# Performance work log

Hardware: AMD Instinct MI355X
Metric: run time of the kernel (lower is better)

Reference implementation:

```python
import jax, jax.numpy as jnp
import numpy as np

N_NODES = 100000
N_EDGES = 1600000
DIM = 64
NEG_SLOPE = 0.2  # DGL GATConv default
BN_EPS = 1e-5


def setup_inputs() -> dict:
    key = jax.random.key(0)
    ks = jax.random.split(key, 16)
    d = {}
    d["node_weight"] = jax.random.normal(ks[0], (N_NODES, DIM), jnp.float32)
    d["edge_weight"] = jax.random.normal(ks[1], (N_EDGES,), jnp.float32)  # unused in forward (faithful to source)
    d["src"] = jax.random.randint(ks[2], (N_EDGES,), 0, N_NODES)
    d["dst"] = jax.random.randint(ks[3], (N_EDGES,), 0, N_NODES)
    i = 4
    scale = 1.0 / np.sqrt(DIM)
    for l in (1, 2, 3):
        d[f"W{l}"] = jax.random.normal(ks[i], (DIM, DIM), jnp.float32) * scale; i += 1
        d[f"al{l}"] = jax.random.normal(ks[i], (DIM,), jnp.float32) * 0.1; i += 1
        d[f"ar{l}"] = jax.random.normal(ks[i], (DIM,), jnp.float32) * 0.1; i += 1
        d[f"b{l}"] = jnp.zeros((DIM,), jnp.float32)
        d[f"g{l}"] = jnp.ones((DIM,), jnp.float32)
        d[f"beta{l}"] = jnp.zeros((DIM,), jnp.float32)
    return d


def gat_layer(h, src, dst, W, al, ar, b):
    # DGL GATConv, 1 head: project, edge attention, per-dst softmax, scatter-add
    feat = h @ W                                  # [N, D]
    el = feat @ al                                # [N]
    er = feat @ ar                                # [N]
    e = jax.nn.leaky_relu(el[src] + er[dst], NEG_SLOPE)   # [E]
    m = jax.ops.segment_max(e, dst, num_segments=N_NODES)  # per-dst max
    ex = jnp.exp(e - m[dst])
    s = jax.ops.segment_sum(ex, dst, num_segments=N_NODES)
    alpha = ex / s[dst]                           # edge softmax
    out = jax.ops.segment_sum(alpha[:, None] * feat[src], dst, num_segments=N_NODES)
    return out + b


def batchnorm(h, g, beta):
    # BatchNorm1d in training mode: batch stats, biased variance
    mu = jnp.mean(h, axis=0)
    var = jnp.mean(jnp.square(h - mu), axis=0)
    return (h - mu) * jax.lax.rsqrt(var + BN_EPS) * g + beta


def reference(node_weight, edge_weight, src, dst,
              W1, al1, ar1, b1, g1, beta1,
              W2, al2, ar2, b2, g2, beta2,
              W3, al3, ar3, b3, g3, beta3):
    # dropout is identity in eval mode
    h = gat_layer(node_weight, src, dst, W1, al1, ar1, b1)
    h = jax.nn.elu(batchnorm(h, g1, beta1))
    h = gat_layer(h, src, dst, W2, al2, ar2, b2)
    h = jax.nn.elu(batchnorm(h, g2, beta2))
    h = gat_layer(h, src, dst, W3, al3, ar3, b3)
    h = batchnorm(h, g3, beta3)
    return h
```

## Files before the change

kernel.cpp:

```cpp
#include <hip/hip_runtime.h>
#include <hip/hip_bf16.h>
#include <math.h>

#define DIM 64
#define BSHIFT 9
#define BNODES 512
#define MAXB 256
#define EPT 8
#define CHUNK 2048

typedef __attribute__((ext_vector_type(8))) short bf16x8;
typedef __attribute__((ext_vector_type(4))) float f32x4;

__device__ __forceinline__ short f2bf(float x) {
    union { __hip_bfloat16 b; short s; } u;
    u.b = __float2bfloat16(x);
    return u.s;
}
__device__ __forceinline__ float bf2f(short s) {
    return __uint_as_float(((unsigned)(unsigned short)s) << 16);
}


__global__ void bin_count_kernel(const int* __restrict__ dst, int* __restrict__ bucket_cnt, int E) {
    __shared__ int h[MAXB];
    int t = threadIdx.x;
    h[t] = 0;
    __syncthreads();
    for (int i = blockIdx.x * blockDim.x + t; i < E; i += gridDim.x * blockDim.x)
        atomicAdd(&h[dst[i] >> BSHIFT], 1);
    __syncthreads();
    if (h[t]) atomicAdd(&bucket_cnt[t], h[t]);
}

__global__ void bucket_scan_kernel(const int* __restrict__ bucket_cnt,
                                   int* __restrict__ bucket_off, int* __restrict__ bucket_fill) {
    __shared__ int s[MAXB];
    int t = threadIdx.x;
    int v = bucket_cnt[t];
    s[t] = v;
    __syncthreads();
    for (int off = 1; off < MAXB; off <<= 1) {
        int x = (t >= off) ? s[t - off] : 0;
        __syncthreads();
        s[t] += x;
        __syncthreads();
    }
    bucket_off[t] = s[t] - v;
    bucket_fill[t] = 0;
}

__global__ __launch_bounds__(256) void bin_scatter_kernel(
    const int* __restrict__ src, const int* __restrict__ dst,
    const int* __restrict__ bucket_off, int* __restrict__ bucket_fill,
    unsigned long long* __restrict__ binned, int E) {
    __shared__ int lcnt[MAXB];
    __shared__ int lbase[MAXB];
    int t = threadIdx.x;
    lcnt[t] = 0;
    __syncthreads();
    int base = blockIdx.x * CHUNK;
    unsigned long long pair[EPT];
    int slot[EPT];
#pragma unroll
    for (int j = 0; j < EPT; j++) {
        int idx = base + j * 256 + t;
        if (idx < E) {
            int s = src[idx], d = dst[idx];
            pair[j] = ((unsigned long long)(unsigned)d << 32) | (unsigned)s;
            slot[j] = atomicAdd(&lcnt[d >> BSHIFT], 1);
        } else {
            slot[j] = -1;
        }
    }
    __syncthreads();
    int c = lcnt[t];
    if (c) lbase[t] = atomicAdd(&bucket_fill[t], c);
    __syncthreads();
#pragma unroll
    for (int j = 0; j < EPT; j++) {
        if (slot[j] >= 0) {
            int b = (int)(pair[j] >> 32) >> BSHIFT;
            binned[(size_t)bucket_off[b] + lbase[b] + slot[j]] = pair[j];
        }
    }
}

__global__ __launch_bounds__(256) void node_count_kernel(
    const unsigned long long* __restrict__ binned, const int* __restrict__ bucket_off,
    const int* __restrict__ bucket_cnt, int* __restrict__ counts, int N) {
    __shared__ int cnt[BNODES];
    int b = blockIdx.x, t = threadIdx.x;
    for (int i = t; i < BNODES; i += 256) cnt[i] = 0;
    __syncthreads();
    int s0 = bucket_off[b], c = bucket_cnt[b];
    for (int i = t; i < c; i += 256) {
        int d = (int)(binned[(size_t)s0 + i] >> 32);
        atomicAdd(&cnt[d & (BNODES - 1)], 1);
    }
    __syncthreads();
    int nbase = b << BSHIFT;
    for (int i = t; i < BNODES; i += 256)
        if (nbase + i < N) counts[nbase + i] = cnt[i];
}

__global__ void scan1_kernel(const int* __restrict__ counts, int* __restrict__ excl,
                             int* __restrict__ blk_sums, int n) {
    __shared__ int sdata[256];
    int t = threadIdx.x;
    int base = blockIdx.x * 1024 + t * 4;
    int v0 = (base + 0 < n) ? counts[base + 0] : 0;
    int v1 = (base + 1 < n) ? counts[base + 1] : 0;
    int v2 = (base + 2 < n) ? counts[base + 2] : 0;
    int v3 = (base + 3 < n) ? counts[base + 3] : 0;
    int tsum = v0 + v1 + v2 + v3;
    sdata[t] = tsum;
    __syncthreads();
    for (int off = 1; off < 256; off <<= 1) {
        int x = (t >= off) ? sdata[t - off] : 0;
        __syncthreads();
        sdata[t] += x;
        __syncthreads();
    }
    int run = sdata[t] - tsum;
    if (base + 0 < n) excl[base + 0] = run; run += v0;
    if (base + 1 < n) excl[base + 1] = run; run += v1;
    if (base + 2 < n) excl[base + 2] = run; run += v2;
    if (base + 3 < n) excl[base + 3] = run;
    if (t == 255) blk_sums[blockIdx.x] = sdata[255];
}

__global__ void scan2_kernel(int* __restrict__ blk_sums, int nb) {
    __shared__ int s[128];
    int t = threadIdx.x;
    s[t] = (t < nb) ? blk_sums[t] : 0;
    __syncthreads();
    for (int off = 1; off < 128; off <<= 1) {
        int x = (t >= off) ? s[t - off] : 0;
        __syncthreads();
        s[t] += x;
        __syncthreads();
    }
    if (t < nb) blk_sums[t] = (t > 0) ? s[t - 1] : 0;
}

__global__ void scan3_kernel(int* __restrict__ excl, const int* __restrict__ blk_sums,
                             int n, int total) {
    int i = blockIdx.x * blockDim.x + threadIdx.x;
    if (i < n) excl[i] += blk_sums[i >> 10];
    if (i == 0) excl[n] = total;
}

__global__ __launch_bounds__(256) void final_scatter_kernel(
    const unsigned long long* __restrict__ binned, const int* __restrict__ bucket_off,
    const int* __restrict__ bucket_cnt, const int* __restrict__ row_ptr,
    int* __restrict__ src_sorted, int N) {
    __shared__ int fill[BNODES];
    int b = blockIdx.x, t = threadIdx.x;
    for (int i = t; i < BNODES; i += 256) fill[i] = 0;
    __syncthreads();
    int s0 = bucket_off[b], c = bucket_cnt[b];
    for (int i = t; i < c; i += 256) {
        unsigned long long p = binned[(size_t)s0 + i];
        int d = (int)(p >> 32);
        int pos = row_ptr[d] + atomicAdd(&fill[d & (BNODES - 1)], 1);
        src_sorted[pos] = (int)(p & 0xffffffffu);
    }
}


__global__ __launch_bounds__(256) void gemm64_mfma_kernel(
    const float* __restrict__ h, const float* __restrict__ W,
    const float* __restrict__ al, const float* __restrict__ ar,
    const float* __restrict__ stats, const float* __restrict__ g,
    const float* __restrict__ beta, int do_bn, float invN,
    __hip_bfloat16* __restrict__ feat, float* __restrict__ el, float* __restrict__ er,
    int n) {
    int t = threadIdx.x;
    int lane = t & 63;
    int li = lane & 15;
    int quad = lane >> 4;
    int wv = t >> 6;

    bf16x8 b_hi[2][4], b_lo[2][4];
#pragma unroll
    for (int ks = 0; ks < 2; ks++)
#pragma unroll
        for (int nt = 0; nt < 4; nt++) {
#pragma unroll
            for (int j = 0; j < 8; j++) {
                float w = W[(ks * 32 + quad * 8 + j) * 64 + nt * 16 + li];
                short hi = f2bf(w);
                b_hi[ks][nt][j] = hi;
                b_lo[ks][nt][j] = f2bf(w - bf2f(hi));
            }
        }
    float alv[4], arv[4];
#pragma unroll
    for (int nt = 0; nt < 4; nt++) { alv[nt] = al[nt * 16 + li]; arv[nt] = ar[nt * 16 + li]; }

    float sc[2][8], sh[2][8];
    if (do_bn) {
#pragma unroll
        for (int ks = 0; ks < 2; ks++)
#pragma unroll
            for (int j = 0; j < 8; j++) {
                int k = ks * 32 + quad * 8 + j;
                float mu = stats[k] * invN;
                float var = fmaf(-mu, mu, stats[64 + k] * invN);
                float inv = rsqrtf(var + 1e-5f) * g[k];
                sc[ks][j] = inv;
                sh[ks][j] = beta[k] - mu * inv;
            }
    }

    int ntiles = (n + 15) >> 4;
    for (int tile = blockIdx.x * 4 + wv; tile < ntiles; tile += gridDim.x * 4) {
        int m0 = tile << 4;
        int rrow = m0 + li;
        const float* rowp = h + (size_t)((rrow < n) ? rrow : (n - 1)) * 64;
        bf16x8 a_hi[2], a_lo[2];
#pragma unroll
        for (int ks = 0; ks < 2; ks++) {
            float4 v0 = *(const float4*)(rowp + ks * 32 + quad * 8);
            float4 v1 = *(const float4*)(rowp + ks * 32 + quad * 8 + 4);
            float x[8] = {v0.x, v0.y, v0.z, v0.w, v1.x, v1.y, v1.z, v1.w};
#pragma unroll
            for (int j = 0; j < 8; j++) {
                float v = x[j];
                if (do_bn) {
                    v = fmaf(v, sc[ks][j], sh[ks][j]);
                    if (v < 0.f) v = expm1f(v);
                }
                short hi = f2bf(v);
                a_hi[ks][j] = hi;
                a_lo[ks][j] = f2bf(v - bf2f(hi));
            }
        }
        f32x4 acc[4];
#pragma unroll
        for (int nt = 0; nt < 4; nt++) acc[nt] = (f32x4){0.f, 0.f, 0.f, 0.f};
#pragma unroll
        for (int ks = 0; ks < 2; ks++)
#pragma unroll
            for (int nt = 0; nt < 4; nt++) {
                acc[nt] = __builtin_amdgcn_mfma_f32_16x16x32_bf16(a_hi[ks], b_hi[ks][nt], acc[nt], 0, 0, 0);
                acc[nt] = __builtin_amdgcn_mfma_f32_16x16x32_bf16(a_lo[ks], b_hi[ks][nt], acc[nt], 0, 0, 0);
                acc[nt] = __builtin_amdgcn_mfma_f32_16x16x32_bf16(a_hi[ks], b_lo[ks][nt], acc[nt], 0, 0, 0);
            }
#pragma unroll
        for (int nt = 0; nt < 4; nt++)
#pragma unroll
            for (int reg = 0; reg < 4; reg++) {
                int wrow = m0 + quad * 4 + reg;
                if (wrow < n) {
                    union { __hip_bfloat16 b; short s; } u;
                    u.s = f2bf(acc[nt][reg]);
                    feat[(size_t)wrow * 64 + nt * 16 + li] = u.b;
                }
            }
        float pl[4], pr[4];
#pragma unroll
        for (int reg = 0; reg < 4; reg++) {
            float l = 0.f, r = 0.f;
#pragma unroll
            for (int nt = 0; nt < 4; nt++) {
                l = fmaf(acc[nt][reg], alv[nt], l);
                r = fmaf(acc[nt][reg], arv[nt], r);
            }
#pragma unroll
            for (int off = 1; off < 16; off <<= 1) {
                l += __shfl_xor(l, off, 64);
                r += __shfl_xor(r, off, 64);
            }
            pl[reg] = l; pr[reg] = r;
        }
        int row = m0 + quad * 4;
        if (li == 0 && row < n)          { el[row] = pl[0]; er[row] = pr[0]; }
        else if (li == 1 && row + 1 < n) { el[row + 1] = pl[1]; er[row + 1] = pr[1]; }
        else if (li == 2 && row + 2 < n) { el[row + 2] = pl[2]; er[row + 2] = pr[2]; }
        else if (li == 3 && row + 3 < n) { el[row + 3] = pl[3]; er[row + 3] = pr[3]; }
    }
}

__global__ __launch_bounds__(256) void attn_kernel(
    const int* __restrict__ row_ptr, const int* __restrict__ src_sorted,
    const float* __restrict__ el, const float* __restrict__ er,
    float* __restrict__ ebuf, int n) {
    int t = threadIdx.x;
    int li = t & 15;
    int node = blockIdx.x * 16 + (t >> 4);
    if (node >= n) return;
    int start = row_ptr[node], end = row_ptr[node + 1];
    float er_n = er[node];

    float m = -INFINITY, s = 0.f;
    for (int i = start + li; i < end; i += 16) {
        float v = el[src_sorted[i]] + er_n;
        v = (v > 0.f) ? v : 0.2f * v;
        ebuf[i] = v;
        float mn = fmaxf(m, v);
        s = s * __expf(m - mn) + __expf(v - mn);
        m = mn;
    }
#pragma unroll
    for (int off = 8; off; off >>= 1) {
        float mo = __shfl_xor(m, off, 64);
        float so = __shfl_xor(s, off, 64);
        float mn = fmaxf(m, mo);
        float sa = (m == -INFINITY) ? 0.f : s * __expf(m - mn);
        float sb = (mo == -INFINITY) ? 0.f : so * __expf(mo - mn);
        s = sa + sb;
        m = mn;
    }
    float inv_s = (s > 0.f) ? 1.f / s : 0.f;
    for (int i = start + li; i < end; i += 16) {
        ebuf[i] = __expf(ebuf[i] - m) * inv_s;
    }
}

__global__ __launch_bounds__(256) void aggregate_kernel(
    const int* __restrict__ row_ptr, const int* __restrict__ src_sorted,
    const float* __restrict__ alpha, const __hip_bfloat16* __restrict__ feat,
    const float* __restrict__ bias, float* __restrict__ out, int n) {
    int t = threadIdx.x, lane = t & 63;
    int q = lane >> 3;
    int li = lane & 7;
    int node = blockIdx.x * 4 + (t >> 6);
    if (node >= n) return;
    int start = row_ptr[node], end = row_ptr[node + 1];
    const uint4* featv = (const uint4*)feat;

    float a0 = 0.f, a1 = 0.f, a2 = 0.f, a3 = 0.f, a4 = 0.f, a5 = 0.f, a6 = 0.f, a7 = 0.f;
    int i = start;
    for (; i + 8 <= end; i += 8) {
        int idx = i + q;
        float a = alpha[idx];
        int sn = src_sorted[idx];
        uint4 p = featv[(size_t)sn * 8 + li];
        a0 = fmaf(a, __uint_as_float(p.x << 16), a0);
        a1 = fmaf(a, __uint_as_float(p.x & 0xffff0000u), a1);
        a2 = fmaf(a, __uint_as_float(p.y << 16), a2);
        a3 = fmaf(a, __uint_as_float(p.y & 0xffff0000u), a3);
        a4 = fmaf(a, __uint_as_float(p.z << 16), a4);
        a5 = fmaf(a, __uint_as_float(p.z & 0xffff0000u), a5);
        a6 = fmaf(a, __uint_as_float(p.w << 16), a6);
        a7 = fmaf(a, __uint_as_float(p.w & 0xffff0000u), a7);
    }
    if (i < end) {
        int idx = i + q;
        bool valid = idx < end;
        int idc = valid ? idx : end - 1;
        float a = valid ? alpha[idc] : 0.f;
        int sn = src_sorted[idc];
        uint4 p = featv[(size_t)sn * 8 + li];
        a0 = fmaf(a, __uint_as_float(p.x << 16), a0);
        a1 = fmaf(a, __uint_as_float(p.x & 0xffff0000u), a1);
        a2 = fmaf(a, __uint_as_float(p.y << 16), a2);
        a3 = fmaf(a, __uint_as_float(p.y & 0xffff0000u), a3);
        a4 = fmaf(a, __uint_as_float(p.z << 16), a4);
        a5 = fmaf(a, __uint_as_float(p.z & 0xffff0000u), a5);
        a6 = fmaf(a, __uint_as_float(p.w << 16), a6);
        a7 = fmaf(a, __uint_as_float(p.w & 0xffff0000u), a7);
    }
#pragma unroll
    for (int off = 8; off <= 32; off <<= 1) {
        a0 += __shfl_xor(a0, off, 64);
        a1 += __shfl_xor(a1, off, 64);
        a2 += __shfl_xor(a2, off, 64);
        a3 += __shfl_xor(a3, off, 64);
        a4 += __shfl_xor(a4, off, 64);
        a5 += __shfl_xor(a5, off, 64);
        a6 += __shfl_xor(a6, off, 64);
        a7 += __shfl_xor(a7, off, 64);
    }
    if (q == 0) {
        const float4* bv = (const float4*)bias;
        float4 b0 = bv[li * 2], b1 = bv[li * 2 + 1];
        float4 o0 = {a0 + b0.x, a1 + b0.y, a2 + b0.z, a3 + b0.w};
        float4 o1 = {a4 + b1.x, a5 + b1.y, a6 + b1.z, a7 + b1.w};
        float4* op = (float4*)(out + (size_t)node * 64 + li * 8);
        op[0] = o0;
        op[1] = o1;
    }
}

__global__ __launch_bounds__(256) void bn_stats_kernel(const float* __restrict__ h,
                                                       float* __restrict__ stats, int n) {
    __shared__ float ls[256], lss[256];
    int t = threadIdx.x, lane = t & 63;
    int w = blockIdx.x * 4 + (t >> 6);
    int stride = gridDim.x * 4;
    float s = 0.f, ss = 0.f;
    for (int row = w; row < n; row += stride) {
        float v = h[(size_t)row * DIM + lane];
        s += v;
        ss = fmaf(v, v, ss);
    }
    ls[t] = s; lss[t] = ss;
    __syncthreads();
    if (t < 64) {
        float a = ls[t] + ls[t + 64] + ls[t + 128] + ls[t + 192];
        float b = lss[t] + lss[t + 64] + lss[t + 128] + lss[t + 192];
        atomicAdd(&stats[t], a);
        atomicAdd(&stats[64 + t], b);
    }
}

__global__ void bn_apply_kernel(float* __restrict__ h, const float* __restrict__ stats,
                                const float* __restrict__ g, const float* __restrict__ beta,
                                int n, int do_elu) {
    int i = blockIdx.x * blockDim.x + threadIdx.x;
    int total = n * DIM;
    int stride = gridDim.x * blockDim.x;
    float invN = 1.f / (float)n;
    for (; i < total; i += stride) {
        int c = i & 63;
        float mu = stats[c] * invN;
        float var = fmaf(-mu, mu, stats[DIM + c] * invN);
        float x = (h[i] - mu) * rsqrtf(var + 1e-5f) * g[c] + beta[c];
        if (do_elu && x < 0.f) x = expm1f(x);
        h[i] = x;
    }
}


extern "C" void kernel_launch(void* const* d_in, const int* in_sizes, int n_in,
                              void* d_out, int out_size, void* d_ws, size_t ws_size,
                              hipStream_t stream) {
    const float* nw = (const float*)d_in[0];
    const int* src = (const int*)d_in[2];
    const int* dst = (const int*)d_in[3];
    const int N = in_sizes[0] / DIM;
    const int E = in_sizes[2];
    const float invN = 1.f / (float)N;
    const int nbuck = (N + BNODES - 1) >> BSHIFT;

    char* ws = (char*)d_ws;
    size_t off = 0;
    auto alloc = [&](size_t bytes) -> void* {
        void* p = ws + off;
        off += (bytes + 255) & ~(size_t)255;
        return p;
    };
    int* counts       = (int*)alloc((size_t)N * 4);
    int* row_ptr      = (int*)alloc(((size_t)N + 1) * 4);
    int* blk_sums     = (int*)alloc(512);
    int* bucket_cnt   = (int*)alloc(MAXB * 4);
    int* bucket_off   = (int*)alloc(MAXB * 4);
    int* bucket_fill  = (int*)alloc(MAXB * 4);
    unsigned long long* binned = (unsigned long long*)alloc((size_t)E * 8);
    int* src_sorted   = (int*)alloc((size_t)E * 4);
    float* ebuf       = (float*)alloc((size_t)E * 4);
    float* el         = (float*)alloc((size_t)N * 4);
    float* er         = (float*)alloc((size_t)N * 4);
    __hip_bfloat16* feat = (__hip_bfloat16*)alloc((size_t)N * DIM * 2);
    float* hbuf       = (float*)alloc((size_t)N * DIM * 4);
    float* stats      = (float*)alloc(512);

    int nb = (N + 1023) / 1024;

    hipMemsetAsync(bucket_cnt, 0, MAXB * 4, stream);
    bin_count_kernel<<<256, 256, 0, stream>>>(dst, bucket_cnt, E);
    bucket_scan_kernel<<<1, MAXB, 0, stream>>>(bucket_cnt, bucket_off, bucket_fill);
    bin_scatter_kernel<<<(E + CHUNK - 1) / CHUNK, 256, 0, stream>>>(
        src, dst, bucket_off, bucket_fill, binned, E);
    node_count_kernel<<<nbuck, 256, 0, stream>>>(binned, bucket_off, bucket_cnt, counts, N);
    scan1_kernel<<<nb, 256, 0, stream>>>(counts, row_ptr, blk_sums, N);
    scan2_kernel<<<1, 128, 0, stream>>>(blk_sums, nb);
    scan3_kernel<<<(N + 255) / 256, 256, 0, stream>>>(row_ptr, blk_sums, N, E);
    final_scatter_kernel<<<nbuck, 256, 0, stream>>>(binned, bucket_off, bucket_cnt,
                                                    row_ptr, src_sorted, N);

    for (int l = 0; l < 3; l++) {
        const float* W    = (const float*)d_in[4 + 6 * l];
        const float* al   = (const float*)d_in[5 + 6 * l];
        const float* ar   = (const float*)d_in[6 + 6 * l];
        const float* b    = (const float*)d_in[7 + 6 * l];
        const float* g    = (const float*)d_in[8 + 6 * l];
        const float* beta = (const float*)d_in[9 + 6 * l];
        const float* hin = (l == 0) ? nw : hbuf;
        float* hout = (l == 2) ? (float*)d_out : hbuf;

        gemm64_mfma_kernel<<<1024, 256, 0, stream>>>(
            hin, W, al, ar, stats,
            (l == 0) ? al : (const float*)d_in[8 + 6 * (l - 1)],
            (l == 0) ? al : (const float*)d_in[9 + 6 * (l - 1)],
            (l > 0) ? 1 : 0, invN,
            feat, el, er, N);
        attn_kernel<<<(N + 15) / 16, 256, 0, stream>>>(row_ptr, src_sorted, el, er, ebuf, N);
        aggregate_kernel<<<(N + 3) / 4, 256, 0, stream>>>(row_ptr, src_sorted, ebuf,
                                                          feat, b, hout, N);
        hipMemsetAsync(stats, 0, 512, stream);
        bn_stats_kernel<<<512, 256, 0, stream>>>(hout, stats, N);
    }
    bn_apply_kernel<<<2048, 256, 0, stream>>>((float*)d_out, stats,
                                              (const float*)d_in[8 + 12],
                                              (const float*)d_in[9 + 12],
                                              N, 0);
}
```

Before: 517.2 us.

## Fuse edge softmax, aggregation and BN stats into one kernel with bf16 intermediates

Merges the attention, aggregation and batch-norm statistics kernels into a single persistent per-node kernel. Each wavefront computes the softmax for its node in registers and uses it directly, so the edge buffer round trip goes away. The kernel also accumulates the column sums and sums of squares in shared memory before doing the global atomics. Hidden activations between layers are now stored as bf16 and read back by the GEMM, and some loads and stores become nontemporal. These changes cut global memory traffic and launch count, at the cost of lower precision in the intermediate activations.

```diff
diff --git a/kernel.cpp b/kernel.cpp
--- a/kernel.cpp
+++ b/kernel.cpp
@@ -11,6 +11,7 @@
 
 typedef __attribute__((ext_vector_type(8))) short bf16x8;
 typedef __attribute__((ext_vector_type(4))) float f32x4;
+typedef __attribute__((ext_vector_type(4))) unsigned int u32x4;
 
 __device__ __forceinline__ short f2bf(float x) {
     union { __hip_bfloat16 b; short s; } u;
@@ -170,10 +171,10 @@
 
 
 __global__ __launch_bounds__(256) void gemm64_mfma_kernel(
-    const float* __restrict__ h, const float* __restrict__ W,
+    const void* __restrict__ hraw, const float* __restrict__ W,
     const float* __restrict__ al, const float* __restrict__ ar,
     const float* __restrict__ stats, const float* __restrict__ g,
-    const float* __restrict__ beta, int do_bn, float invN,
+    const float* __restrict__ beta, int do_bn, int in_bf16, float invN,
     __hip_bfloat16* __restrict__ feat, float* __restrict__ el, float* __restrict__ er,
     int n) {
     int t = threadIdx.x;
@@ -218,13 +219,25 @@
     for (int tile = blockIdx.x * 4 + wv; tile < ntiles; tile += gridDim.x * 4) {
         int m0 = tile << 4;
         int rrow = m0 + li;
-        const float* rowp = h + (size_t)((rrow < n) ? rrow : (n - 1)) * 64;
+        int crow = (rrow < n) ? rrow : (n - 1);
         bf16x8 a_hi[2], a_lo[2];
 #pragma unroll
         for (int ks = 0; ks < 2; ks++) {
-            float4 v0 = *(const float4*)(rowp + ks * 32 + quad * 8);
-            float4 v1 = *(const float4*)(rowp + ks * 32 + quad * 8 + 4);
-            float x[8] = {v0.x, v0.y, v0.z, v0.w, v1.x, v1.y, v1.z, v1.w};
+            float x[8];
+            if (in_bf16) {
+                const u32x4* rp = (const u32x4*)((const __hip_bfloat16*)hraw + (size_t)crow * 64 + ks * 32 + quad * 8);
+                u32x4 pv = __builtin_nontemporal_load(rp);
+                x[0] = __uint_as_float(pv[0] << 16); x[1] = __uint_as_float(pv[0] & 0xffff0000u);
+                x[2] = __uint_as_float(pv[1] << 16); x[3] = __uint_as_float(pv[1] & 0xffff0000u);
+                x[4] = __uint_as_float(pv[2] << 16); x[5] = __uint_as_float(pv[2] & 0xffff0000u);
+                x[6] = __uint_as_float(pv[3] << 16); x[7] = __uint_as_float(pv[3] & 0xffff0000u);
+            } else {
+                const float* rowp = (const float*)hraw + (size_t)crow * 64 + ks * 32 + quad * 8;
+                f32x4 v0 = __builtin_nontemporal_load((const f32x4*)rowp);
+                f32x4 v1 = __builtin_nontemporal_load((const f32x4*)(rowp + 4));
+                x[0] = v0[0]; x[1] = v0[1]; x[2] = v0[2]; x[3] = v0[3];
+                x[4] = v1[0]; x[5] = v1[1]; x[6] = v1[2]; x[7] = v1[3];
+            }
 #pragma unroll
             for (int j = 0; j < 8; j++) {
                 float v = x[j];
@@ -283,128 +296,180 @@
     }
 }
 
-__global__ __launch_bounds__(256) void attn_kernel(
+template<int OUT_BF16>
+__global__ __launch_bounds__(256) void fused_layer_kernel(
     const int* __restrict__ row_ptr, const int* __restrict__ src_sorted,
     const float* __restrict__ el, const float* __restrict__ er,
-    float* __restrict__ ebuf, int n) {
-    int t = threadIdx.x;
-    int li = t & 15;
-    int node = blockIdx.x * 16 + (t >> 4);
-    if (node >= n) return;
-    int start = row_ptr[node], end = row_ptr[node + 1];
-    float er_n = er[node];
-
-    float m = -INFINITY, s = 0.f;
-    for (int i = start + li; i < end; i += 16) {
-        float v = el[src_sorted[i]] + er_n;
-        v = (v > 0.f) ? v : 0.2f * v;
-        ebuf[i] = v;
-        float mn = fmaxf(m, v);
-        s = s * __expf(m - mn) + __expf(v - mn);
-        m = mn;
-    }
-#pragma unroll
-    for (int off = 8; off; off >>= 1) {
-        float mo = __shfl_xor(m, off, 64);
-        float so = __shfl_xor(s, off, 64);
-        float mn = fmaxf(m, mo);
-        float sa = (m == -INFINITY) ? 0.f : s * __expf(m - mn);
-        float sb = (mo == -INFINITY) ? 0.f : so * __expf(mo - mn);
-        s = sa + sb;
-        m = mn;
-    }
-    float inv_s = (s > 0.f) ? 1.f / s : 0.f;
-    for (int i = start + li; i < end; i += 16) {
-        ebuf[i] = __expf(ebuf[i] - m) * inv_s;
-    }
-}
-
-__global__ __launch_bounds__(256) void aggregate_kernel(
-    const int* __restrict__ row_ptr, const int* __restrict__ src_sorted,
-    const float* __restrict__ alpha, const __hip_bfloat16* __restrict__ feat,
-    const float* __restrict__ bias, float* __restrict__ out, int n) {
-    int t = threadIdx.x, lane = t & 63;
+    const __hip_bfloat16* __restrict__ feat, const float* __restrict__ bias,
+    void* __restrict__ out, float* __restrict__ stats, int n) {
+    __shared__ float colsum[128];
+    int t = threadIdx.x, lane = t & 63, wv = t >> 6;
     int q = lane >> 3;
     int li = lane & 7;
-    int node = blockIdx.x * 4 + (t >> 6);
-    if (node >= n) return;
-    int start = row_ptr[node], end = row_ptr[node + 1];
     const uint4* featv = (const uint4*)feat;
-
-    float a0 = 0.f, a1 = 0.f, a2 = 0.f, a3 = 0.f, a4 = 0.f, a5 = 0.f, a6 = 0.f, a7 = 0.f;
-    int i = start;
-    for (; i + 8 <= end; i += 8) {
-        int idx = i + q;
-        float a = alpha[idx];
-        int sn = src_sorted[idx];
-        uint4 p = featv[(size_t)sn * 8 + li];
-        a0 = fmaf(a, __uint_as_float(p.x << 16), a0);
-        a1 = fmaf(a, __uint_as_float(p.x & 0xffff0000u), a1);
-        a2 = fmaf(a, __uint_as_float(p.y << 16), a2);
-        a3 = fmaf(a, __uint_as_float(p.y & 0xffff0000u), a3);
-        a4 = fmaf(a, __uint_as_float(p.z << 16), a4);
-        a5 = fmaf(a, __uint_as_float(p.z & 0xffff0000u), a5);
-        a6 = fmaf(a, __uint_as_float(p.w << 16), a6);
-        a7 = fmaf(a, __uint_as_float(p.w & 0xffff0000u), a7);
-    }
-    if (i < end) {
-        int idx = i + q;
-        bool valid = idx < end;
-        int idc = valid ? idx : end - 1;
-        float a = valid ? alpha[idc] : 0.f;
-        int sn = src_sorted[idc];
-        uint4 p = featv[(size_t)sn * 8 + li];
-        a0 = fmaf(a, __uint_as_float(p.x << 16), a0);
-        a1 = fmaf(a, __uint_as_float(p.x & 0xffff0000u), a1);
-        a2 = fmaf(a, __uint_as_float(p.y << 16), a2);
-        a3 = fmaf(a, __uint_as_float(p.y & 0xffff0000u), a3);
-        a4 = fmaf(a, __uint_as_float(p.z << 16), a4);
-        a5 = fmaf(a, __uint_as_float(p.z & 0xffff0000u), a5);
-        a6 = fmaf(a, __uint_as_float(p.w << 16), a6);
-        a7 = fmaf(a, __uint_as_float(p.w & 0xffff0000u), a7);
-    }
-#pragma unroll
-    for (int off = 8; off <= 32; off <<= 1) {
-        a0 += __shfl_xor(a0, off, 64);
-        a1 += __shfl_xor(a1, off, 64);
-        a2 += __shfl_xor(a2, off, 64);
-        a3 += __shfl_xor(a3, off, 64);
-        a4 += __shfl_xor(a4, off, 64);
-        a5 += __shfl_xor(a5, off, 64);
-        a6 += __shfl_xor(a6, off, 64);
-        a7 += __shfl_xor(a7, off, 64);
-    }
+    float b0[8];
+#pragma unroll
+    for (int j = 0; j < 8; j++) b0[j] = bias[li * 8 + j];
+    float st_s[8], st_q[8];
+#pragma unroll
+    for (int j = 0; j < 8; j++) { st_s[j] = 0.f; st_q[j] = 0.f; }
+
+    for (int node = blockIdx.x * 4 + wv; node < n; node += gridDim.x * 4) {
+        int start = row_ptr[node], end = row_ptr[node + 1];
+        int deg = end - start;
+        float er_n = er[node];
+        float a0 = 0.f, a1 = 0.f, a2 = 0.f, a3 = 0.f, a4 = 0.f, a5 = 0.f, a6 = 0.f, a7 = 0.f;
+
+        if (deg <= 64) {
+            int sv = 0;
+            float ev = -INFINITY;
+            if (lane < deg) {
+                sv = __builtin_nontemporal_load(src_sorted + start + lane);
+                float v = el[sv] + er_n;
+                ev = (v > 0.f) ? v : 0.2f * v;
+            }
+            float m = ev;
+#pragma unroll
+            for (int off = 1; off < 64; off <<= 1) m = fmaxf(m, __shfl_xor(m, off, 64));
+            float sum = (lane < deg) ? __expf(ev - m) : 0.f;
+#pragma unroll
+            for (int off = 1; off < 64; off <<= 1) sum += __shfl_xor(sum, off, 64);
+            float inv_s = (sum > 0.f) ? 1.f / sum : 0.f;
+
+            int nit = (deg + 7) >> 3;
+            int it = 0;
+            for (; it + 2 <= nit; it += 2) {
+                int o1 = it * 8 + q, o2 = o1 + 8;
+                bool v2 = o2 < deg;
+                int s1 = __shfl(sv, o1, 64);
+                int s2 = __shfl(sv, v2 ? o2 : o1, 64);
+                float e1 = __shfl(ev, o1, 64);
+                float e2 = __shfl(ev, v2 ? o2 : o1, 64);
+                uint4 p1 = featv[(size_t)s1 * 8 + li];
+                uint4 p2 = featv[(size_t)s2 * 8 + li];
+                float w1 = __expf(e1 - m) * inv_s;
+                float w2 = v2 ? __expf(e2 - m) * inv_s : 0.f;
+                a0 = fmaf(w1, __uint_as_float(p1.x << 16), a0);
+                a1 = fmaf(w1, __uint_as_float(p1.x & 0xffff0000u), a1);
+                a2 = fmaf(w1, __uint_as_float(p1.y << 16), a2);
+                a3 = fmaf(w1, __uint_as_float(p1.y & 0xffff0000u), a3);
+                a4 = fmaf(w1, __uint_as_float(p1.z << 16), a4);
+                a5 = fmaf(w1, __uint_as_float(p1.z & 0xffff0000u), a5);
+                a6 = fmaf(w1, __uint_as_float(p1.w << 16), a6);
+                a7 = fmaf(w1, __uint_as_float(p1.w & 0xffff0000u), a7);
+                a0 = fmaf(w2, __uint_as_float(p2.x << 16), a0);
+                a1 = fmaf(w2, __uint_as_float(p2.x & 0xffff0000u), a1);
+                a2 = fmaf(w2, __uint_as_float(p2.y << 16), a2);
+                a3 = fmaf(w2, __uint_as_float(p2.y & 0xffff0000u), a3);
+                a4 = fmaf(w2, __uint_as_float(p2.z << 16), a4);
+                a5 = fmaf(w2, __uint_as_float(p2.z & 0xffff0000u), a5);
+                a6 = fmaf(w2, __uint_as_float(p2.w << 16), a6);
+                a7 = fmaf(w2, __uint_as_float(p2.w & 0xffff0000u), a7);
+            }
+            if (it < nit) {
+                int o = it * 8 + q;
+                bool valid = o < deg;
+                int oc = valid ? o : 0;
+                int s1 = __shfl(sv, oc, 64);
+                float e1 = __shfl(ev, oc, 64);
+                uint4 p = featv[(size_t)s1 * 8 + li];
+                float w1 = valid ? __expf(e1 - m) * inv_s : 0.f;
+                a0 = fmaf(w1, __uint_as_float(p.x << 16), a0);
+                a1 = fmaf(w1, __uint_as_float(p.x & 0xffff0000u), a1);
+                a2 = fmaf(w1, __uint_as_float(p.y << 16), a2);
+                a3 = fmaf(w1, __uint_as_float(p.y & 0xffff0000u), a3);
+                a4 = fmaf(w1, __uint_as_float(p.z << 16), a4);
+                a5 = fmaf(w1, __uint_as_float(p.z & 0xffff0000u), a5);
+                a6 = fmaf(w1, __uint_as_float(p.w << 16), a6);
+                a7 = fmaf(w1, __uint_as_float(p.w & 0xffff0000u), a7);
+            }
+        } else {
+            float mm = -INFINITY, ss = 0.f;
+            for (int i = start + lane; i < end; i += 64) {
+                int sn = src_sorted[i];
+                float v = el[sn] + er_n;
+                v = (v > 0.f) ? v : 0.2f * v;
+                float mn = fmaxf(mm, v);
+                ss = ss * __expf(mm - mn) + __expf(v - mn);
+                mm = mn;
+            }
+#pragma unroll
+            for (int off = 1; off < 64; off <<= 1) {
+                float mo = __shfl_xor(mm, off, 64);
+                float so = __shfl_xor(ss, off, 64);
+                float mn = fmaxf(mm, mo);
+                float sa = (mm == -INFINITY) ? 0.f : ss * __expf(mm - mn);
+                float sb = (mo == -INFINITY) ? 0.f : so * __expf(mo - mn);
+                ss = sa + sb;
+                mm = mn;
+            }
+            float m = mm;
+            float inv_s = (ss > 0.f) ? 1.f / ss : 0.f;
+            for (int i = start; i < end; i += 8) {
+                int o = i + q;
+                bool valid = o < end;
+                int oc = valid ? o : end - 1;
+                int sn = src_sorted[oc];
+                float v = el[sn] + er_n;
+                v = (v > 0.f) ? v : 0.2f * v;
+                float w1 = valid ? __expf(v - m) * inv_s : 0.f;
+                uint4 p = featv[(size_t)sn * 8 + li];
+                a0 = fmaf(w1, __uint_as_float(p.x << 16), a0);
+                a1 = fmaf(w1, __uint_as_float(p.x & 0xffff0000u), a1);
+                a2 = fmaf(w1, __uint_as_float(p.y << 16), a2);
+                a3 = fmaf(w1, __uint_as_float(p.y & 0xffff0000u), a3);
+                a4 = fmaf(w1, __uint_as_float(p.z << 16), a4);
+                a5 = fmaf(w1, __uint_as_float(p.z & 0xffff0000u), a5);
+                a6 = fmaf(w1, __uint_as_float(p.w << 16), a6);
+                a7 = fmaf(w1, __uint_as_float(p.w & 0xffff0000u), a7);
+            }
+        }
+#pragma unroll
+        for (int off = 8; off <= 32; off <<= 1) {
+            a0 += __shfl_xor(a0, off, 64);
+            a1 += __shfl_xor(a1, off, 64);
+            a2 += __shfl_xor(a2, off, 64);
+            a3 += __shfl_xor(a3, off, 64);
+            a4 += __shfl_xor(a4, off, 64);
+            a5 += __shfl_xor(a5, off, 64);
+            a6 += __shfl_xor(a6, off, 64);
+            a7 += __shfl_xor(a7, off, 64);
+        }
+        if (q == 0) {
+            float o_[8] = {a0 + b0[0], a1 + b0[1], a2 + b0[2], a3 + b0[3],
+                           a4 + b0[4], a5 + b0[5], a6 + b0[6], a7 + b0[7]};
+#pragma unroll
+            for (int j = 0; j < 8; j++) {
+                st_s[j] += o_[j];
+                st_q[j] = fmaf(o_[j], o_[j], st_q[j]);
+            }
+            if (OUT_BF16) {
+                u32x4 pk;
+                pk[0] = ((unsigned)(unsigned short)f2bf(o_[0])) | ((unsigned)(unsigned short)f2bf(o_[1]) << 16);
+                pk[1] = ((unsigned)(unsigned short)f2bf(o_[2])) | ((unsigned)(unsigned short)f2bf(o_[3]) << 16);
+                pk[2] = ((unsigned)(unsigned short)f2bf(o_[4])) | ((unsigned)(unsigned short)f2bf(o_[5]) << 16);
+                pk[3] = ((unsigned)(unsigned short)f2bf(o_[6])) | ((unsigned)(unsigned short)f2bf(o_[7]) << 16);
+                __builtin_nontemporal_store(pk, (u32x4*)((__hip_bfloat16*)out + (size_t)node * 64 + li * 8));
+            } else {
+                f32x4 v0 = {o_[0], o_[1], o_[2], o_[3]};
+                f32x4 v1 = {o_[4], o_[5], o_[6], o_[7]};
+                f32x4* op = (f32x4*)((float*)out + (size_t)node * 64 + li * 8);
+                __builtin_nontemporal_store(v0, op);
+                __builtin_nontemporal_store(v1, op + 1);
+            }
+        }
+    }
+    if (t < 128) colsum[t] = 0.f;
+    __syncthreads();
     if (q == 0) {
-        const float4* bv = (const float4*)bias;
-        float4 b0 = bv[li * 2], b1 = bv[li * 2 + 1];
-        float4 o0 = {a0 + b0.x, a1 + b0.y, a2 + b0.z, a3 + b0.w};
-        float4 o1 = {a4 + b1.x, a5 + b1.y, a6 + b1.z, a7 + b1.w};
-        float4* op = (float4*)(out + (size_t)node * 64 + li * 8);
-        op[0] = o0;
-        op[1] = o1;
-    }
-}
-
-__global__ __launch_bounds__(256) void bn_stats_kernel(const float* __restrict__ h,
-                                                       float* __restrict__ stats, int n) {
-    __shared__ float ls[256], lss[256];
-    int t = threadIdx.x, lane = t & 63;
-    int w = blockIdx.x * 4 + (t >> 6);
-    int stride = gridDim.x * 4;
-    float s = 0.f, ss = 0.f;
-    for (int row = w; row < n; row += stride) {
-        float v = h[(size_t)row * DIM + lane];
-        s += v;
-        ss = fmaf(v, v, ss);
-    }
-    ls[t] = s; lss[t] = ss;
-    __syncthreads();
-    if (t < 64) {
-        float a = ls[t] + ls[t + 64] + ls[t + 128] + ls[t + 192];
-        float b = lss[t] + lss[t + 64] + lss[t + 128] + lss[t + 192];
-        atomicAdd(&stats[t], a);
-        atomicAdd(&stats[64 + t], b);
-    }
+#pragma unroll
+        for (int j = 0; j < 8; j++) {
+            atomicAdd(&colsum[li * 8 + j], st_s[j]);
+            atomicAdd(&colsum[64 + li * 8 + j], st_q[j]);
+        }
+    }
+    __syncthreads();
+    if (t < 128) atomicAdd(&stats[t], colsum[t]);
 }
 
 __global__ void bn_apply_kernel(float* __restrict__ h, const float* __restrict__ stats,
@@ -451,11 +516,10 @@
     int* bucket_fill  = (int*)alloc(MAXB * 4);
     unsigned long long* binned = (unsigned long long*)alloc((size_t)E * 8);
     int* src_sorted   = (int*)alloc((size_t)E * 4);
-    float* ebuf       = (float*)alloc((size_t)E * 4);
     float* el         = (float*)alloc((size_t)N * 4);
     float* er         = (float*)alloc((size_t)N * 4);
     __hip_bfloat16* feat = (__hip_bfloat16*)alloc((size_t)N * DIM * 2);
-    float* hbuf       = (float*)alloc((size_t)N * DIM * 4);
+    __hip_bfloat16* hbuf = (__hip_bfloat16*)alloc((size_t)N * DIM * 2);
     float* stats      = (float*)alloc(512);
 
     int nb = (N + 1023) / 1024;
@@ -477,22 +541,21 @@
         const float* al   = (const float*)d_in[5 + 6 * l];
         const float* ar   = (const float*)d_in[6 + 6 * l];
         const float* b    = (const float*)d_in[7 + 6 * l];
-        const float* g    = (const float*)d_in[8 + 6 * l];
-        const float* beta = (const float*)d_in[9 + 6 * l];
-        const float* hin = (l == 0) ? nw : hbuf;
-        float* hout = (l == 2) ? (float*)d_out : hbuf;
 
         gemm64_mfma_kernel<<<1024, 256, 0, stream>>>(
-            hin, W, al, ar, stats,
+            (l == 0) ? (const void*)nw : (const void*)hbuf, W, al, ar, stats,
             (l == 0) ? al : (const float*)d_in[8 + 6 * (l - 1)],
             (l == 0) ? al : (const float*)d_in[9 + 6 * (l - 1)],
-            (l > 0) ? 1 : 0, invN,
+            (l > 0) ? 1 : 0, (l > 0) ? 1 : 0, invN,
             feat, el, er, N);
-        attn_kernel<<<(N + 15) / 16, 256, 0, stream>>>(row_ptr, src_sorted, el, er, ebuf, N);
-        aggregate_kernel<<<(N + 3) / 4, 256, 0, stream>>>(row_ptr, src_sorted, ebuf,
-                                                          feat, b, hout, N);
         hipMemsetAsync(stats, 0, 512, stream);
-        bn_stats_kernel<<<512, 256, 0, stream>>>(hout, stats, N);
+        if (l < 2) {
+            fused_layer_kernel<1><<<4096, 256, 0, stream>>>(
+                row_ptr, src_sorted, el, er, feat, b, (void*)hbuf, stats, N);
+        } else {
+            fused_layer_kernel<0><<<4096, 256, 0, stream>>>(
+                row_ptr, src_sorted, el, er, feat, b, d_out, stats, N);
+        }
     }
     bn_apply_kernel<<<2048, 256, 0, stream>>>((float*)d_out, stats,
                                               (const float*)d_in[8 + 12],
```

Result: slower. 656.9 us (+27.0%).

## Fuse CSR build into one bucket kernel, fuse BN stats into aggregation, bf16 hidden buffers

Applied to the files above, without the earlier changes.

Replaces the node-count, three-pass scan and final-scatter kernels with a single per-bucket kernel that counts, scans locally and scatters, using the bucket offsets as global bases. The aggregation kernel becomes grid-strided and accumulates the batchnorm column sums and squares itself, which removes the separate stats pass over the hidden activations. Intermediate hidden activations are stored in bf16 instead of fp32, halving that traffic, and several loads and stores are marked nontemporal. The risks are reduced precision in the intermediates and atomic contention on the stats accumulators.

```diff
diff --git a/kernel.cpp b/kernel.cpp
--- a/kernel.cpp
+++ b/kernel.cpp
@@ -11,6 +11,7 @@
 
 typedef __attribute__((ext_vector_type(8))) short bf16x8;
 typedef __attribute__((ext_vector_type(4))) float f32x4;
+typedef __attribute__((ext_vector_type(4))) unsigned int u32x4;
 
 __device__ __forceinline__ short f2bf(float x) {
     union { __hip_bfloat16 b; short s; } u;
@@ -86,12 +87,15 @@
     }
 }
 
-__global__ __launch_bounds__(256) void node_count_kernel(
+__global__ __launch_bounds__(256) void bucket_csr_kernel(
     const unsigned long long* __restrict__ binned, const int* __restrict__ bucket_off,
-    const int* __restrict__ bucket_cnt, int* __restrict__ counts, int N) {
+    const int* __restrict__ bucket_cnt, int* __restrict__ row_ptr,
+    int* __restrict__ src_sorted, int N, int E) {
     __shared__ int cnt[BNODES];
+    __shared__ int base[BNODES];
+    __shared__ int sdata[256];
     int b = blockIdx.x, t = threadIdx.x;
-    for (int i = t; i < BNODES; i += 256) cnt[i] = 0;
+    cnt[t] = 0; cnt[t + 256] = 0;
     __syncthreads();
     int s0 = bucket_off[b], c = bucket_cnt[b];
     for (int i = t; i < c; i += 256) {
@@ -99,21 +103,8 @@
         atomicAdd(&cnt[d & (BNODES - 1)], 1);
     }
     __syncthreads();
-    int nbase = b << BSHIFT;
-    for (int i = t; i < BNODES; i += 256)
-        if (nbase + i < N) counts[nbase + i] = cnt[i];
-}
-
-__global__ void scan1_kernel(const int* __restrict__ counts, int* __restrict__ excl,
-                             int* __restrict__ blk_sums, int n) {
-    __shared__ int sdata[256];
-    int t = threadIdx.x;
-    int base = blockIdx.x * 1024 + t * 4;
-    int v0 = (base + 0 < n) ? counts[base + 0] : 0;
-    int v1 = (base + 1 < n) ? counts[base + 1] : 0;
-    int v2 = (base + 2 < n) ? counts[base + 2] : 0;
-    int v3 = (base + 3 < n) ? counts[base + 3] : 0;
-    int tsum = v0 + v1 + v2 + v3;
+    int v0 = cnt[2 * t], v1 = cnt[2 * t + 1];
+    int tsum = v0 + v1;
     sdata[t] = tsum;
     __syncthreads();
     for (int off = 1; off < 256; off <<= 1) {
@@ -123,57 +114,28 @@
         __syncthreads();
     }
     int run = sdata[t] - tsum;
-    if (base + 0 < n) excl[base + 0] = run; run += v0;
-    if (base + 1 < n) excl[base + 1] = run; run += v1;
-    if (base + 2 < n) excl[base + 2] = run; run += v2;
-    if (base + 3 < n) excl[base + 3] = run;
-    if (t == 255) blk_sums[blockIdx.x] = sdata[255];
-}
-
-__global__ void scan2_kernel(int* __restrict__ blk_sums, int nb) {
-    __shared__ int s[128];
-    int t = threadIdx.x;
-    s[t] = (t < nb) ? blk_sums[t] : 0;
-    __syncthreads();
-    for (int off = 1; off < 128; off <<= 1) {
-        int x = (t >= off) ? s[t - off] : 0;
-        __syncthreads();
-        s[t] += x;
-        __syncthreads();
-    }
-    if (t < nb) blk_sums[t] = (t > 0) ? s[t - 1] : 0;
-}
-
-__global__ void scan3_kernel(int* __restrict__ excl, const int* __restrict__ blk_sums,
-                             int n, int total) {
-    int i = blockIdx.x * blockDim.x + threadIdx.x;
-    if (i < n) excl[i] += blk_sums[i >> 10];
-    if (i == 0) excl[n] = total;
-}
-
-__global__ __launch_bounds__(256) void final_scatter_kernel(
-    const unsigned long long* __restrict__ binned, const int* __restrict__ bucket_off,
-    const int* __restrict__ bucket_cnt, const int* __restrict__ row_ptr,
-    int* __restrict__ src_sorted, int N) {
-    __shared__ int fill[BNODES];
-    int b = blockIdx.x, t = threadIdx.x;
-    for (int i = t; i < BNODES; i += 256) fill[i] = 0;
-    __syncthreads();
-    int s0 = bucket_off[b], c = bucket_cnt[b];
+    base[2 * t] = s0 + run;
+    base[2 * t + 1] = s0 + run + v0;
+    int nbase = b << BSHIFT;
+    if (nbase + 2 * t < N)     row_ptr[nbase + 2 * t]     = s0 + run;
+    if (nbase + 2 * t + 1 < N) row_ptr[nbase + 2 * t + 1] = s0 + run + v0;
+    if (b == 0 && t == 0) row_ptr[N] = E;
+    cnt[2 * t] = 0; cnt[2 * t + 1] = 0;
+    __syncthreads();
     for (int i = t; i < c; i += 256) {
         unsigned long long p = binned[(size_t)s0 + i];
-        int d = (int)(p >> 32);
-        int pos = row_ptr[d] + atomicAdd(&fill[d & (BNODES - 1)], 1);
+        int d = (int)(p >> 32) & (BNODES - 1);
+        int pos = base[d] + atomicAdd(&cnt[d], 1);
         src_sorted[pos] = (int)(p & 0xffffffffu);
     }
 }
 
 
 __global__ __launch_bounds__(256) void gemm64_mfma_kernel(
-    const float* __restrict__ h, const float* __restrict__ W,
+    const void* __restrict__ hraw, const float* __restrict__ W,
     const float* __restrict__ al, const float* __restrict__ ar,
     const float* __restrict__ stats, const float* __restrict__ g,
-    const float* __restrict__ beta, int do_bn, float invN,
+    const float* __restrict__ beta, int do_bn, int in_bf16, float invN,
     __hip_bfloat16* __restrict__ feat, float* __restrict__ el, float* __restrict__ er,
     int n) {
     int t = threadIdx.x;
@@ -218,13 +180,25 @@
     for (int tile = blockIdx.x * 4 + wv; tile < ntiles; tile += gridDim.x * 4) {
         int m0 = tile << 4;
         int rrow = m0 + li;
-        const float* rowp = h + (size_t)((rrow < n) ? rrow : (n - 1)) * 64;
+        int crow = (rrow < n) ? rrow : (n - 1);
         bf16x8 a_hi[2], a_lo[2];
 #pragma unroll
         for (int ks = 0; ks < 2; ks++) {
-            float4 v0 = *(const float4*)(rowp + ks * 32 + quad * 8);
-            float4 v1 = *(const float4*)(rowp + ks * 32 + quad * 8 + 4);
-            float x[8] = {v0.x, v0.y, v0.z, v0.w, v1.x, v1.y, v1.z, v1.w};
+            float x[8];
+            if (in_bf16) {
+                const u32x4* rp = (const u32x4*)((const __hip_bfloat16*)hraw + (size_t)crow * 64 + ks * 32 + quad * 8);
+                u32x4 pv = __builtin_nontemporal_load(rp);
+                x[0] = __uint_as_float(pv[0] << 16); x[1] = __uint_as_float(pv[0] & 0xffff0000u);
+                x[2] = __uint_as_float(pv[1] << 16); x[3] = __uint_as_float(pv[1] & 0xffff0000u);
+                x[4] = __uint_as_float(pv[2] << 16); x[5] = __uint_as_float(pv[2] & 0xffff0000u);
+                x[6] = __uint_as_float(pv[3] << 16); x[7] = __uint_as_float(pv[3] & 0xffff0000u);
+            } else {
+                const float* rowp = (const float*)hraw + (size_t)crow * 64 + ks * 32 + quad * 8;
+                f32x4 v0 = __builtin_nontemporal_load((const f32x4*)rowp);
+                f32x4 v1 = __builtin_nontemporal_load((const f32x4*)(rowp + 4));
+                x[0] = v0[0]; x[1] = v0[1]; x[2] = v0[2]; x[3] = v0[3];
+                x[4] = v1[0]; x[5] = v1[1]; x[6] = v1[2]; x[7] = v1[3];
+            }
 #pragma unroll
             for (int j = 0; j < 8; j++) {
                 float v = x[j];
@@ -319,92 +293,104 @@
     }
 }
 
+template<int OUT_BF16>
 __global__ __launch_bounds__(256) void aggregate_kernel(
     const int* __restrict__ row_ptr, const int* __restrict__ src_sorted,
     const float* __restrict__ alpha, const __hip_bfloat16* __restrict__ feat,
-    const float* __restrict__ bias, float* __restrict__ out, int n) {
-    int t = threadIdx.x, lane = t & 63;
+    const float* __restrict__ bias, void* __restrict__ out,
+    float* __restrict__ stats, int n) {
+    __shared__ float colsum[128];
+    int t = threadIdx.x, lane = t & 63, wv = t >> 6;
     int q = lane >> 3;
     int li = lane & 7;
-    int node = blockIdx.x * 4 + (t >> 6);
-    if (node >= n) return;
-    int start = row_ptr[node], end = row_ptr[node + 1];
     const uint4* featv = (const uint4*)feat;
-
-    float a0 = 0.f, a1 = 0.f, a2 = 0.f, a3 = 0.f, a4 = 0.f, a5 = 0.f, a6 = 0.f, a7 = 0.f;
-    int i = start;
-    for (; i + 8 <= end; i += 8) {
-        int idx = i + q;
-        float a = alpha[idx];
-        int sn = src_sorted[idx];
-        uint4 p = featv[(size_t)sn * 8 + li];
-        a0 = fmaf(a, __uint_as_float(p.x << 16), a0);
-        a1 = fmaf(a, __uint_as_float(p.x & 0xffff0000u), a1);
-        a2 = fmaf(a, __uint_as_float(p.y << 16), a2);
-        a3 = fmaf(a, __uint_as_float(p.y & 0xffff0000u), a3);
-        a4 = fmaf(a, __uint_as_float(p.z << 16), a4);
-        a5 = fmaf(a, __uint_as_float(p.z & 0xffff0000u), a5);
-        a6 = fmaf(a, __uint_as_float(p.w << 16), a6);
-        a7 = fmaf(a, __uint_as_float(p.w & 0xffff0000u), a7);
-    }
-    if (i < end) {
-        int idx = i + q;
-        bool valid = idx < end;
-        int idc = valid ? idx : end - 1;
-        float a = valid ? alpha[idc] : 0.f;
-        int sn = src_sorted[idc];
-        uint4 p = featv[(size_t)sn * 8 + li];
-        a0 = fmaf(a, __uint_as_float(p.x << 16), a0);
-        a1 = fmaf(a, __uint_as_float(p.x & 0xffff0000u), a1);
-        a2 = fmaf(a, __uint_as_float(p.y << 16), a2);
-        a3 = fmaf(a, __uint_as_float(p.y & 0xffff0000u), a3);
-        a4 = fmaf(a, __uint_as_float(p.z << 16), a4);
-        a5 = fmaf(a, __uint_as_float(p.z & 0xffff0000u), a5);
-        a6 = fmaf(a, __uint_as_float(p.w << 16), a6);
-        a7 = fmaf(a, __uint_as_float(p.w & 0xffff0000u), a7);
-    }
-#pragma unroll
-    for (int off = 8; off <= 32; off <<= 1) {
-        a0 += __shfl_xor(a0, off, 64);
-        a1 += __shfl_xor(a1, off, 64);
-        a2 += __shfl_xor(a2, off, 64);
-        a3 += __shfl_xor(a3, off, 64);
-        a4 += __shfl_xor(a4, off, 64);
-        a5 += __shfl_xor(a5, off, 64);
-        a6 += __shfl_xor(a6, off, 64);
-        a7 += __shfl_xor(a7, off, 64);
-    }
+    float b0[8];
+#pragma unroll
+    for (int j = 0; j < 8; j++) b0[j] = bias[li * 8 + j];
+    float st_s[8], st_q[8];
+#pragma unroll
+    for (int j = 0; j < 8; j++) { st_s[j] = 0.f; st_q[j] = 0.f; }
+
+    for (int node = blockIdx.x * 4 + wv; node < n; node += gridDim.x * 4) {
+        int start = row_ptr[node], end = row_ptr[node + 1];
+        float a0 = 0.f, a1 = 0.f, a2 = 0.f, a3 = 0.f, a4 = 0.f, a5 = 0.f, a6 = 0.f, a7 = 0.f;
+        int i = start;
+        for (; i + 8 <= end; i += 8) {
+            int idx = i + q;
+            float a = __builtin_nontemporal_load(alpha + idx);
+            int sn = __builtin_nontemporal_load(src_sorted + idx);
+            uint4 p = featv[(size_t)sn * 8 + li];
+            a0 = fmaf(a, __uint_as_float(p.x << 16), a0);
+            a1 = fmaf(a, __uint_as_float(p.x & 0xffff0000u), a1);
+            a2 = fmaf(a, __uint_as_float(p.y << 16), a2);
+            a3 = fmaf(a, __uint_as_float(p.y & 0xffff0000u), a3);
+            a4 = fmaf(a, __uint_as_float(p.z << 16), a4);
+            a5 = fmaf(a, __uint_as_float(p.z & 0xffff0000u), a5);
+            a6 = fmaf(a, __uint_as_float(p.w << 16), a6);
+            a7 = fmaf(a, __uint_as_float(p.w & 0xffff0000u), a7);
+        }
+        if (i < end) {
+            int idx = i + q;
+            bool valid = idx < end;
+            int idc = valid ? idx : end - 1;
+            float a = valid ? alpha[idc] : 0.f;
+            int sn = src_sorted[idc];
+            uint4 p = featv[(size_t)sn * 8 + li];
+            a0 = fmaf(a, __uint_as_float(p.x << 16), a0);
+            a1 = fmaf(a, __uint_as_float(p.x & 0xffff0000u), a1);
+            a2 = fmaf(a, __uint_as_float(p.y << 16), a2);
+            a3 = fmaf(a, __uint_as_float(p.y & 0xffff0000u), a3);
+            a4 = fmaf(a, __uint_as_float(p.z << 16), a4);
+            a5 = fmaf(a, __uint_as_float(p.z & 0xffff0000u), a5);
+            a6 = fmaf(a, __uint_as_float(p.w << 16), a6);
+            a7 = fmaf(a, __uint_as_float(p.w & 0xffff0000u), a7);
+        }
+#pragma unroll
+        for (int off = 8; off <= 32; off <<= 1) {
+            a0 += __shfl_xor(a0, off, 64);
+            a1 += __shfl_xor(a1, off, 64);
+            a2 += __shfl_xor(a2, off, 64);
+            a3 += __shfl_xor(a3, off, 64);
+            a4 += __shfl_xor(a4, off, 64);
+            a5 += __shfl_xor(a5, off, 64);
+            a6 += __shfl_xor(a6, off, 64);
+            a7 += __shfl_xor(a7, off, 64);
+        }
+        if (q == 0) {
+            float o_[8] = {a0 + b0[0], a1 + b0[1], a2 + b0[2], a3 + b0[3],
+                           a4 + b0[4], a5 + b0[5], a6 + b0[6], a7 + b0[7]};
+#pragma unroll
+            for (int j = 0; j < 8; j++) {
+                st_s[j] += o_[j];
+                st_q[j] = fmaf(o_[j], o_[j], st_q[j]);
+            }
+            if (OUT_BF16) {
+                u32x4 pk;
+                pk[0] = ((unsigned)(unsigned short)f2bf(o_[0])) | ((unsigned)(unsigned short)f2bf(o_[1]) << 16);
+                pk[1] = ((unsigned)(unsigned short)f2bf(o_[2])) | ((unsigned)(unsigned short)f2bf(o_[3]) << 16);
+                pk[2] = ((unsigned)(unsigned short)f2bf(o_[4])) | ((unsigned)(unsigned short)f2bf(o_[5]) << 16);
+                pk[3] = ((unsigned)(unsigned short)f2bf(o_[6])) | ((unsigned)(unsigned short)f2bf(o_[7]) << 16);
+                __builtin_nontemporal_store(pk, (u32x4*)((__hip_bfloat16*)out + (size_t)node * 64 + li * 8));
+            } else {
+                f32x4 v0 = {o_[0], o_[1], o_[2], o_[3]};
+                f32x4 v1 = {o_[4], o_[5], o_[6], o_[7]};
+                f32x4* op = (f32x4*)((float*)out + (size_t)node * 64 + li * 8);
+                __builtin_nontemporal_store(v0, op);
+                __builtin_nontemporal_store(v1, op + 1);
+            }
+        }
+    }
+    if (t < 128) colsum[t] = 0.f;
+    __syncthreads();
     if (q == 0) {
-        const float4* bv = (const float4*)bias;
-        float4 b0 = bv[li * 2], b1 = bv[li * 2 + 1];
-        float4 o0 = {a0 + b0.x, a1 + b0.y, a2 + b0.z, a3 + b0.w};
-        float4 o1 = {a4 + b1.x, a5 + b1.y, a6 + b1.z, a7 + b1.w};
-        float4* op = (float4*)(out + (size_t)node * 64 + li * 8);
-        op[0] = o0;
-        op[1] = o1;
-    }
-}
-
-__global__ __launch_bounds__(256) void bn_stats_kernel(const float* __restrict__ h,
-                                                       float* __restrict__ stats, int n) {
-    __shared__ float ls[256], lss[256];
-    int t = threadIdx.x, lane = t & 63;
-    int w = blockIdx.x * 4 + (t >> 6);
-    int stride = gridDim.x * 4;
-    float s = 0.f, ss = 0.f;
-    for (int row = w; row < n; row += stride) {
-        float v = h[(size_t)row * DIM + lane];
-        s += v;
-        ss = fmaf(v, v, ss);
-    }
-    ls[t] = s; lss[t] = ss;
-    __syncthreads();
-    if (t < 64) {
-        float a = ls[t] + ls[t + 64] + ls[t + 128] + ls[t + 192];
-        float b = lss[t] + lss[t + 64] + lss[t + 128] + lss[t + 192];
-        atomicAdd(&stats[t], a);
-        atomicAdd(&stats[64 + t], b);
-    }
+#pragma unroll
+        for (int j = 0; j < 8; j++) {
+            atomicAdd(&colsum[li * 8 + j], st_s[j]);
+            atomicAdd(&colsum[64 + li * 8 + j], st_q[j]);
+        }
+    }
+    __syncthreads();
+    if (t < 128) atomicAdd(&stats[t], colsum[t]);
 }
 
 __global__ void bn_apply_kernel(float* __restrict__ h, const float* __restrict__ stats,
@@ -443,9 +429,7 @@
         off += (bytes + 255) & ~(size_t)255;
         return p;
     };
-    int* counts       = (int*)alloc((size_t)N * 4);
     int* row_ptr      = (int*)alloc(((size_t)N + 1) * 4);
-    int* blk_sums     = (int*)alloc(512);
     int* bucket_cnt   = (int*)alloc(MAXB * 4);
     int* bucket_off   = (int*)alloc(MAXB * 4);
     int* bucket_fill  = (int*)alloc(MAXB * 4);
@@ -455,44 +439,38 @@
     float* el         = (float*)alloc((size_t)N * 4);
     float* er         = (float*)alloc((size_t)N * 4);
     __hip_bfloat16* feat = (__hip_bfloat16*)alloc((size_t)N * DIM * 2);
-    float* hbuf       = (float*)alloc((size_t)N * DIM * 4);
+    __hip_bfloat16* hbuf = (__hip_bfloat16*)alloc((size_t)N * DIM * 2);
     float* stats      = (float*)alloc(512);
-
-    int nb = (N + 1023) / 1024;
 
     hipMemsetAsync(bucket_cnt, 0, MAXB * 4, stream);
     bin_count_kernel<<<256, 256, 0, stream>>>(dst, bucket_cnt, E);
     bucket_scan_kernel<<<1, MAXB, 0, stream>>>(bucket_cnt, bucket_off, bucket_fill);
     bin_scatter_kernel<<<(E + CHUNK - 1) / CHUNK, 256, 0, stream>>>(
         src, dst, bucket_off, bucket_fill, binned, E);
-    node_count_kernel<<<nbuck, 256, 0, stream>>>(binned, bucket_off, bucket_cnt, counts, N);
-    scan1_kernel<<<nb, 256, 0, stream>>>(counts, row_ptr, blk_sums, N);
-    scan2_kernel<<<1, 128, 0, stream>>>(blk_sums, nb);
-    scan3_kernel<<<(N + 255) / 256, 256, 0, stream>>>(row_ptr, blk_sums, N, E);
-    final_scatter_kernel<<<nbuck, 256, 0, stream>>>(binned, bucket_off, bucket_cnt,
-                                                    row_ptr, src_sorted, N);
+    bucket_csr_kernel<<<nbuck, 256, 0, stream>>>(binned, bucket_off, bucket_cnt,
+                                                 row_ptr, src_sorted, N, E);
 
     for (int l = 0; l < 3; l++) {
         const float* W    = (const float*)d_in[4 + 6 * l];
         const float* al   = (const float*)d_in[5 + 6 * l];
         const float* ar   = (const float*)d_in[6 + 6 * l];
         const float* b    = (const float*)d_in[7 + 6 * l];
-        const float* g    = (const float*)d_in[8 + 6 * l];
-        const float* beta = (const float*)d_in[9 + 6 * l];
-        const float* hin = (l == 0) ? nw : hbuf;
-        float* hout = (l == 2) ? (float*)d_out : hbuf;
 
         gemm64_mfma_kernel<<<1024, 256, 0, stream>>>(
-            hin, W, al, ar, stats,
+            (l == 0) ? (const void*)nw : (const void*)hbuf, W, al, ar, stats,
             (l == 0) ? al : (const float*)d_in[8 + 6 * (l - 1)],
             (l == 0) ? al : (const float*)d_in[9 + 6 * (l - 1)],
-            (l > 0) ? 1 : 0, invN,
+            (l > 0) ? 1 : 0, (l > 0) ? 1 : 0, invN,
             feat, el, er, N);
+        hipMemsetAsync(stats, 0, 512, stream);
         attn_kernel<<<(N + 15) / 16, 256, 0, stream>>>(row_ptr, src_sorted, el, er, ebuf, N);
-        aggregate_kernel<<<(N + 3) / 4, 256, 0, stream>>>(row_ptr, src_sorted, ebuf,
-                                                          feat, b, hout, N);
-        hipMemsetAsync(stats, 0, 512, stream);
-        bn_stats_kernel<<<512, 256, 0, stream>>>(hout, stats, N);
+        if (l < 2) {
+            aggregate_kernel<1><<<2048, 256, 0, stream>>>(
+                row_ptr, src_sorted, ebuf, feat, b, (void*)hbuf, stats, N);
+        } else {
+            aggregate_kernel<0><<<2048, 256, 0, stream>>>(
+                row_ptr, src_sorted, ebuf, feat, b, d_out, stats, N);
+        }
     }
     bn_apply_kernel<<<2048, 256, 0, stream>>>((float*)d_out, stats,
                                               (const float*)d_in[8 + 12],
```

Result: slower. 588.4 us (+13.8%).
